# Kernel optimization log

Hardware: AMD Instinct MI355X
Metric: run time of the kernel (lower is better)

## Reference

```python
import jax, jax.numpy as jnp
import numpy as np

# ---- dims (match init_kwargs) ----
D_MODEL = 512
N_HEADS = 8
EXPAND = 2
SHRINK = 1
BATCH = 8
SEQ = 4096            # == tno_max_l
DPB_DIM = 512         # dpb_embedding
D1 = EXPAND * D_MODEL                 # 1024 (u_proj / o1 out)
D2 = D_MODEL // SHRINK                # 512  (v_proj out)
HEAD_DIM = D2 // N_HEADS              # 64
EPS = 1e-8


def _srms(x, d):
    # SimpleRMSNorm: x / (||x||_2 * d^-0.5 + eps)
    norm = jnp.linalg.norm(x, axis=-1, keepdims=True)
    return x / (norm * (d ** -0.5) + EPS)


def _dpb(p, Wp, bp, W1, b1, W2, b2, W3, b3):
    # dynamic position bias MLP: scalar rel-pos -> h*head_dim kernel coeffs
    x = p @ Wp + bp
    x = jax.nn.relu(_srms(x, DPB_DIM)) @ W1 + b1
    x = jax.nn.relu(_srms(x, DPB_DIM)) @ W2 + b2
    x = jax.nn.relu(_srms(x, DPB_DIM)) @ W3 + b3
    return x  # (m, h*head_dim)


def _heads(k):
    # (m, h*d) -> (h, m, d)
    return k.reshape(-1, N_HEADS, HEAD_DIM).transpose(1, 0, 2)


def setup_inputs() -> dict:
    key = jax.random.key(0)
    ks = jax.random.split(key, 17)
    w = lambda k, shape: jax.random.normal(k, shape, dtype=jnp.float32) * 0.02
    return {
        "x": jax.random.normal(ks[0], (BATCH, SEQ, D_MODEL), dtype=jnp.float32),
        "Wu": w(ks[1], (D_MODEL, D1)), "bu": w(ks[2], (D1,)),
        "Wv": w(ks[3], (D_MODEL, D2)), "bv": w(ks[4], (D2,)),
        "Wo1": w(ks[5], (D2, D1)), "bo1": w(ks[6], (D1,)),
        "Wo2": w(ks[7], (D1, D_MODEL)), "bo2": w(ks[8], (D_MODEL,)),
        "dpb_Wp": w(ks[9], (1, DPB_DIM)), "dpb_bp": w(ks[10], (DPB_DIM,)),
        "dpb_W1": w(ks[11], (DPB_DIM, DPB_DIM)), "dpb_b1": w(ks[12], (DPB_DIM,)),
        "dpb_W2": w(ks[13], (DPB_DIM, DPB_DIM)), "dpb_b2": w(ks[14], (DPB_DIM,)),
        "dpb_W3": w(ks[15], (DPB_DIM, N_HEADS * HEAD_DIM)),
        "dpb_b3": w(ks[16], (N_HEADS * HEAD_DIM,)),
    }


def reference(x, Wu, bu, Wv, bv, Wo1, bo1, Wo2, bo2,
              dpb_Wp, dpb_bp, dpb_W1, dpb_b1, dpb_W2, dpb_b2, dpb_W3, dpb_b3):
    b, n, _ = x.shape
    shortcut = x
    xn = _srms(x, D2)                                  # pre_norm (SimpleRMSNorm(d2))
    u = jax.nn.silu(xn @ Wu + bu)                      # (b, n, d1)
    v = jax.nn.silu(xn @ Wv + bv)                      # (b, n, d2)
    v = v.reshape(b, n, N_HEADS, HEAD_DIM).transpose(0, 2, 1, 3)  # (b, h, n, d)

    # relative-position indices (par_type=1): 1..n-1, -(n-1)..-1, 0
    pos_idx = jnp.arange(1, n, dtype=jnp.float32)[:, None]   # (n-1, 1)
    neg_idx = -pos_idx[::-1]                                  # (n-1, 1)
    zero_idx = jnp.zeros((1, 1), jnp.float32)
    dpb = lambda p: _dpb(p, dpb_Wp, dpb_bp, dpb_W1, dpb_b1,
                         dpb_W2, dpb_b2, dpb_W3, dpb_b3)
    kz = _heads(dpb(zero_idx))   # (h, 1,   d)
    kp = _heads(dpb(pos_idx))    # (h, n-1, d)
    kn = _heads(dpb(neg_idx))    # (h, n-1, d)
    # circulant embedding of the Toeplitz kernel: [t0, t1..t{n-1}, 0, t{-(n-1)}..t{-1}]
    a = jnp.concatenate([kz, kp, kz, kn], axis=1)             # (h, 2n, d)

    m = 2 * n
    yf = jnp.fft.rfft(v, m, axis=-2)                          # (b, h, n+1, d) complex
    af = jnp.fft.rfft(a, m, axis=-2)[None]                    # (1, h, n+1, d)
    out = jnp.fft.irfft(yf * af, m, axis=-2)[..., :n, :]      # (b, h, n, d)

    out = out.transpose(0, 2, 1, 3).reshape(b, n, D2)         # b n (h d)
    out = (out @ Wo1 + bo1) * u                               # gate
    out = out @ Wo2 + bo2 + shortcut
    return out
```

## Files before the change

kernel.cpp:

```cpp
#include <hip/hip_runtime.h>
#include <hip/hip_fp16.h>


#define FFTN 8192
#define SWZ(p) ((p) ^ (((p) >> 8) & 31))

#define C45F 0.70710678118654752f
#define CC8F 0.92387953251128676f
#define SS8F 0.38268343236508977f

typedef unsigned short u16;
typedef unsigned int u32;
typedef __attribute__((ext_vector_type(8))) short bf16x8;
typedef __attribute__((ext_vector_type(4))) float f32x4;

__device__ __forceinline__ int brev13(int x) { return (int)(__brev((unsigned)x) >> 19); }
__device__ __forceinline__ float b2f(u16 u) {
  union { float f; u32 i; } c; c.i = ((u32)u) << 16; return c.f;
}
__device__ __forceinline__ u16 f2b(float f) {
  union { float f; u32 i; } c; c.f = f;
  u32 r = c.i + 0x7FFFu + ((c.i >> 16) & 1u);
  return (u16)(r >> 16);
}
__device__ __forceinline__ float silu_f(float x) { return x / (1.f + __expf(-x)); }

__device__ __forceinline__ float2 up2(u32 v) {
  __half2 h = __builtin_bit_cast(__half2, v);
  return make_float2(__low2float(h), __high2float(h));
}
__device__ __forceinline__ u32 dn2(float r, float i) {
  __half2 h = __floats2half2_rn(r, i);
  return __builtin_bit_cast(u32, h);
}

__device__ __forceinline__ void gload16(const void* g, void* l) {
  __builtin_amdgcn_global_load_lds(
      (const __attribute__((address_space(1))) u32*)g,
      (__attribute__((address_space(3))) u32*)l, 16, 0, 0);
}

__global__ void twiddle_init_kernel(float2* __restrict__ tw) {
  int k = blockIdx.x * blockDim.x + threadIdx.x;
  if (k < 4096) {
    double ang = -6.283185307179586476925286766559 * ((double)k / 8192.0);
    tw[k] = make_float2((float)cos(ang), (float)sin(ang));
  }
}

__global__ __launch_bounds__(256) void srms_bf16_kernel(
    const float* __restrict__ in, u16* __restrict__ out, int rows, int do_relu)
{
  int wave = threadIdx.x >> 6, lane = threadIdx.x & 63;
  int row = (blockIdx.x << 2) + wave;
  if (row >= rows) return;
  const float4* p = (const float4*)(in + (size_t)row * 512);
  float4 a = p[lane], b = p[lane + 64];
  float ss = a.x*a.x + a.y*a.y + a.z*a.z + a.w*a.w
           + b.x*b.x + b.y*b.y + b.z*b.z + b.w*b.w;
#pragma unroll
  for (int off = 32; off > 0; off >>= 1) ss += __shfl_xor(ss, off);
  float inv = 1.0f / (sqrtf(ss) * 0.04419417382415922f + 1e-8f);
  a.x *= inv; a.y *= inv; a.z *= inv; a.w *= inv;
  b.x *= inv; b.y *= inv; b.z *= inv; b.w *= inv;
  if (do_relu) {
    a.x = fmaxf(a.x, 0.f); a.y = fmaxf(a.y, 0.f); a.z = fmaxf(a.z, 0.f); a.w = fmaxf(a.w, 0.f);
    b.x = fmaxf(b.x, 0.f); b.y = fmaxf(b.y, 0.f); b.z = fmaxf(b.z, 0.f); b.w = fmaxf(b.w, 0.f);
  }
  u16* o = out + (size_t)row * 512;
  ushort4 s0, s1;
  s0.x = f2b(a.x); s0.y = f2b(a.y); s0.z = f2b(a.z); s0.w = f2b(a.w);
  s1.x = f2b(b.x); s1.y = f2b(b.y); s1.z = f2b(b.z); s1.w = f2b(b.w);
  *(ushort4*)(o + lane * 4) = s0;
  *(ushort4*)(o + 256 + lane * 4) = s1;
}

__global__ __launch_bounds__(256) void dpb0_kernel(
    const float* __restrict__ Wp, const float* __restrict__ bp, u16* __restrict__ out)
{
  int wave = threadIdx.x >> 6, lane = threadIdx.x & 63;
  int row = (blockIdx.x << 2) + wave;
  if (row >= 8192) return;
  float pv;
  if (row == 0 || row == 4096) pv = 0.f;
  else if (row < 4096) pv = (float)row;
  else pv = (float)(row - 8192);
  const float4* wp  = (const float4*)Wp;
  const float4* bpp = (const float4*)bp;
  float4 a = wp[lane], b = wp[lane + 64];
  float4 c = bpp[lane], d = bpp[lane + 64];
  a.x = fmaf(pv, a.x, c.x); a.y = fmaf(pv, a.y, c.y);
  a.z = fmaf(pv, a.z, c.z); a.w = fmaf(pv, a.w, c.w);
  b.x = fmaf(pv, b.x, d.x); b.y = fmaf(pv, b.y, d.y);
  b.z = fmaf(pv, b.z, d.z); b.w = fmaf(pv, b.w, d.w);
  float ss = a.x*a.x + a.y*a.y + a.z*a.z + a.w*a.w
           + b.x*b.x + b.y*b.y + b.z*b.z + b.w*b.w;
#pragma unroll
  for (int off = 32; off > 0; off >>= 1) ss += __shfl_xor(ss, off);
  float inv = 1.0f / (sqrtf(ss) * 0.04419417382415922f + 1e-8f);
  u16* o = out + (size_t)row * 512;
  ushort4 s0, s1;
  s0.x = f2b(fmaxf(a.x * inv, 0.f)); s0.y = f2b(fmaxf(a.y * inv, 0.f));
  s0.z = f2b(fmaxf(a.z * inv, 0.f)); s0.w = f2b(fmaxf(a.w * inv, 0.f));
  s1.x = f2b(fmaxf(b.x * inv, 0.f)); s1.y = f2b(fmaxf(b.y * inv, 0.f));
  s1.z = f2b(fmaxf(b.z * inv, 0.f)); s1.w = f2b(fmaxf(b.w * inv, 0.f));
  *(ushort4*)(o + lane * 4) = s0;
  *(ushort4*)(o + 256 + lane * 4) = s1;
}

__global__ __launch_bounds__(256) void wtrans_kernel(
    const float* __restrict__ in, u16* __restrict__ out, int R, int C)
{
  __shared__ float tile[32][33];
  const int c0 = blockIdx.x << 5, r0 = blockIdx.y << 5;
  const int tx = threadIdx.x, ty = threadIdx.y;
#pragma unroll
  for (int i = 0; i < 32; i += 8)
    tile[ty + i][tx] = in[(size_t)(r0 + ty + i) * C + c0 + tx];
  __syncthreads();
#pragma unroll
  for (int i = 0; i < 32; i += 8)
    out[(size_t)(c0 + ty + i) * R + r0 + tx] = f2b(tile[tx][ty + i]);
}

__global__ __launch_bounds__(256) void transpose_b16_kernel(
    const u16* __restrict__ in, u16* __restrict__ out)
{
  __shared__ u16 tile[32][33];
  const int b = blockIdx.z;
  const int j0 = blockIdx.x << 5, c0 = blockIdx.y << 5;
  const int tx = threadIdx.x, ty = threadIdx.y;
  const u16* ip = in + ((size_t)b << 21);
  u16* op = out + ((size_t)b << 21);
#pragma unroll
  for (int i = 0; i < 32; i += 8)
    tile[ty + i][tx] = ip[(size_t)(c0 + ty + i) * 4096 + j0 + tx];
  __syncthreads();
#pragma unroll
  for (int i = 0; i < 32; i += 8)
    op[(size_t)(j0 + ty + i) * 512 + c0 + tx] = tile[tx][ty + i];
}

template <int EPI>
__global__ __launch_bounds__(256) void gemm_bf16_kernel(
    const u16* __restrict__ A, const u16* __restrict__ Bt,
    const float* __restrict__ bias, const u16* __restrict__ aux16,
    const float* __restrict__ auxf, void* __restrict__ Cv,
    int M, int N, int K)
{
  __shared__ __align__(16) u16 As[4096];
  __shared__ __align__(16) u16 Bs[4096];
  const int tid = threadIdx.x;
  const int lane = tid & 63;
  const int w = tid >> 6;
  const int wm = (w >> 1) << 6;
  const int wn = (w & 1) << 6;
  const int lm = lane & 15;
  const int lq = lane >> 4;
  const int bm = blockIdx.y << 7;
  const int bn = blockIdx.x << 7;

  const int sm = tid & 127;
  const int sk = tid >> 7;
  const u16* Ap = A + (size_t)(bm + sm) * K + sk * 8;
  const u16* Bp = Bt + (size_t)(bn + sm) * K + sk * 8;
  u16* As0 = As + ((sk)     * 128 + sm) * 8;
  u16* As1 = As + ((2 + sk) * 128 + sm) * 8;
  u16* Bs0 = Bs + ((sk)     * 128 + sm) * 8;
  u16* Bs1 = Bs + ((2 + sk) * 128 + sm) * 8;

  f32x4 acc[4][4];
#pragma unroll
  for (int i = 0; i < 4; i++)
#pragma unroll
    for (int j = 0; j < 4; j++) acc[i][j] = (f32x4){0.f, 0.f, 0.f, 0.f};

  for (int k0 = 0; k0 < K; k0 += 32) {
    __syncthreads();
    gload16(Ap, As0); gload16(Ap + 16, As1);
    gload16(Bp, Bs0); gload16(Bp + 16, Bs1);
    Ap += 32; Bp += 32;
    __builtin_amdgcn_s_waitcnt(0);
    __syncthreads();
    bf16x8 af[4], bfr[4];
#pragma unroll
    for (int i = 0; i < 4; i++) {
      af[i]  = *(const bf16x8*)(As + (lq * 128 + wm + i * 16 + lm) * 8);
      bfr[i] = *(const bf16x8*)(Bs + (lq * 128 + wn + i * 16 + lm) * 8);
    }
#pragma unroll
    for (int i = 0; i < 4; i++)
#pragma unroll
      for (int j = 0; j < 4; j++)
        acc[i][j] = __builtin_amdgcn_mfma_f32_16x16x32_bf16(af[i], bfr[j], acc[i][j], 0, 0, 0);
  }

#pragma unroll
  for (int i = 0; i < 4; i++) {
    const int m0 = bm + wm + i * 16 + lq * 4;
#pragma unroll
    for (int j = 0; j < 4; j++) {
      const int n = bn + wn + j * 16 + lm;
      const float bb = bias[n];
      const f32x4 v = acc[i][j];
      if constexpr (EPI == 5) {
        float4 o = make_float4(v[0] + bb, v[1] + bb, v[2] + bb, v[3] + bb);
        *(float4*)((float*)Cv + (size_t)n * M + m0) = o;
      } else {
#pragma unroll
        for (int r = 0; r < 4; r++) {
          const size_t idx = (size_t)(m0 + r) * N + n;
          const float val = v[r] + bb;
          if constexpr (EPI == 0) ((float*)Cv)[idx] = val;
          if constexpr (EPI == 1) ((u16*)Cv)[idx] = f2b(silu_f(val));
          if constexpr (EPI == 3) ((u16*)Cv)[idx] = f2b(val * b2f(aux16[idx]));
          if constexpr (EPI == 4) ((float*)Cv)[idx] = val + auxf[idx];
        }
      }
    }
  }
}

template <int EPI>
__global__ __launch_bounds__(512, 1) void gemm256_bf16_kernel(
    const u16* __restrict__ A, const u16* __restrict__ Bt,
    const float* __restrict__ bias, const u16* __restrict__ aux16,
    const float* __restrict__ auxf, void* __restrict__ Cv,
    int M, int N, int K)
{
  __shared__ __align__(16) u16 Asm[2][16384];
  __shared__ __align__(16) u16 Bsm[2][16384];
  const int tid = threadIdx.x;
  const int lane = tid & 63;
  const int w = tid >> 6;
  const int wm = (w >> 2) << 7;
  const int wn = (w & 3) << 6;
  const int lm = lane & 15;
  const int lq = lane >> 4;
  const int bm = blockIdx.y << 8;
  const int bn = blockIdx.x << 8;

  const int rloc = tid & 127;
  const int kq0 = tid >> 7;
  const u16* Ag = A + (size_t)(bm + rloc) * K + kq0 * 8;
  const u16* Bg = Bt + (size_t)(bn + rloc) * K + kq0 * 8;
  const size_t hstep = (size_t)128 * K;
  const int lso = tid * 8;

  const int aBase = ((wm >> 7) * 8192) + lq * 1024 + lm * 8;

  f32x4 acc[8][4];
#pragma unroll
  for (int i = 0; i < 8; i++)
#pragma unroll
    for (int j = 0; j < 4; j++) acc[i][j] = (f32x4){0.f, 0.f, 0.f, 0.f};

#define STG256(gb, lb, hh, kt) do {                                       \
    const u16* g_ = (gb) + (size_t)(hh) * hstep + (size_t)(kt) * 64;      \
    u16* l_ = (lb) + (hh) * 8192 + lso;                                   \
    gload16(g_, l_); gload16(g_ + 32, l_ + 4096);                         \
  } while (0)

  STG256(Ag, &Asm[0][0], 0, 0); STG256(Ag, &Asm[0][0], 1, 0);
  STG256(Bg, &Bsm[0][0], 0, 0); STG256(Bg, &Bsm[0][0], 1, 0);

  const int NT = K >> 6;
  for (int t = 0; t < NT; ++t) {
    const int cb = t & 1, nb = cb ^ 1;
    const u16* cA = &Asm[cb][0];
    const u16* cB = &Bsm[cb][0];
    if (t + 1 < NT) {
      STG256(Ag, &Asm[nb][0], 0, t + 1);
      STG256(Ag, &Asm[nb][0], 1, t + 1);
      asm volatile("s_waitcnt vmcnt(4)" ::: "memory");
    } else {
      asm volatile("s_waitcnt vmcnt(0)" ::: "memory");
    }
    __builtin_amdgcn_s_barrier();
    bf16x8 af[4][2];
#pragma unroll
    for (int q = 0; q < 4; ++q) {
      const int qm = q >> 1, qn = q & 1;
      if (q == 0 && t + 1 < NT) STG256(Bg, &Bsm[nb][0], 0, t + 1);
      if (q == 1 && t + 1 < NT) STG256(Bg, &Bsm[nb][0], 1, t + 1);
      if (qn == 0) {
#pragma unroll
        for (int i = 0; i < 4; ++i)
#pragma unroll
          for (int ks = 0; ks < 2; ++ks)
            af[i][ks] = *(const bf16x8*)(cA + aBase + ks * 4096 + qm * 512 + i * 128);
      }
      const int colBase = wn + qn * 32;
      const int bBase = ((colBase >> 7) * 8192) + lq * 1024 + (colBase & 127) * 8 + lm * 8;
      bf16x8 bfr[2][2];
#pragma unroll
      for (int j = 0; j < 2; ++j)
#pragma unroll
        for (int ks = 0; ks < 2; ++ks)
          bfr[j][ks] = *(const bf16x8*)(cB + bBase + ks * 4096 + j * 128);
      __builtin_amdgcn_s_setprio(1);
#pragma unroll
      for (int i = 0; i < 4; ++i)
#pragma unroll
        for (int j = 0; j < 2; ++j) {
          acc[qm*4+i][qn*2+j] = __builtin_amdgcn_mfma_f32_16x16x32_bf16(
              af[i][0], bfr[j][0], acc[qm*4+i][qn*2+j], 0, 0, 0);
          acc[qm*4+i][qn*2+j] = __builtin_amdgcn_mfma_f32_16x16x32_bf16(
              af[i][1], bfr[j][1], acc[qm*4+i][qn*2+j], 0, 0, 0);
        }
      __builtin_amdgcn_s_setprio(0);
      __builtin_amdgcn_s_barrier();
    }
  }
#undef STG256

#pragma unroll
  for (int im = 0; im < 8; im++) {
    const int m0 = bm + wm + im * 16 + lq * 4;
#pragma unroll
    for (int jn = 0; jn < 4; jn++) {
      const int n = bn + wn + jn * 16 + lm;
      const float bb = bias[n];
      const f32x4 v = acc[im][jn];
      if constexpr (EPI == 2) {
        const int b = m0 >> 12;
        const int jq = m0 & 4095;
        ushort4 s;
        s.x = f2b(silu_f(v[0] + bb)); s.y = f2b(silu_f(v[1] + bb));
        s.z = f2b(silu_f(v[2] + bb)); s.w = f2b(silu_f(v[3] + bb));
        *(ushort4*)((u16*)Cv + (((size_t)(b * 512 + n)) << 12) + jq) = s;
      } else {
#pragma unroll
        for (int r = 0; r < 4; r++) {
          const size_t idx = (size_t)(m0 + r) * N + n;
          const float val = v[r] + bb;
          if constexpr (EPI == 1) ((u16*)Cv)[idx] = f2b(silu_f(val));
          if constexpr (EPI == 3) ((u16*)Cv)[idx] = f2b(val * b2f(aux16[idx]));
          if constexpr (EPI == 4) ((float*)Cv)[idx] = val + auxf[idx];
        }
      }
    }
  }
}

__device__ __forceinline__ void fft8192_dit(float* sr, float* si,
                                            const float2* __restrict__ tw)
{
  const int t = threadIdx.x;
  for (int s = 0; s < 12; s += 2) {
    __syncthreads();
    const int h = 1 << s;
#pragma unroll
    for (int bb = 0; bb < 4; bb++) {
      const int u = t + (bb << 9);
      const int j = u & (h - 1);
      const int base = ((u >> s) << (s + 2)) | j;
      const float2 w1 = tw[j << (12 - s)];
      const float2 w2 = tw[j << (11 - s)];
      const int q0 = SWZ(base), q1 = SWZ(base + h);
      const int q2 = SWZ(base + 2 * h), q3 = SWZ(base + 3 * h);
      const float ar = sr[q0], ai = si[q0];
      const float br = sr[q1], bi = si[q1];
      const float cr = sr[q2], ci = si[q2];
      const float dr = sr[q3], di = si[q3];
      const float t1r = br * w1.x - bi * w1.y, t1i = br * w1.y + bi * w1.x;
      const float t2r = dr * w1.x - di * w1.y, t2i = dr * w1.y + di * w1.x;
      const float Ar = ar + t1r, Ai = ai + t1i;
      const float Br = ar - t1r, Bi = ai - t1i;
      const float Cr = cr + t2r, Ci = ci + t2i;
      const float Dr = cr - t2r, Di = ci - t2i;
      const float t3r = Cr * w2.x - Ci * w2.y, t3i = Cr * w2.y + Ci * w2.x;
      const float pr  = Dr * w2.x - Di * w2.y, pi  = Dr * w2.y + Di * w2.x;
      const float t4r = pi, t4i = -pr;
      sr[q0] = Ar + t3r; si[q0] = Ai + t3i;
      sr[q2] = Ar - t3r; si[q2] = Ai - t3i;
      sr[q1] = Br + t4r; si[q1] = Bi + t4i;
      sr[q3] = Br - t4r; si[q3] = Bi - t4i;
    }
  }
  __syncthreads();
#pragma unroll
  for (int bb = 0; bb < 8; bb++) {
    const int u = t + (bb << 9);
    const float2 w = tw[u];
    const int p0 = SWZ(u), p1 = SWZ(u + 4096);
    const float br = sr[p1], bi = si[p1];
    const float trr = br * w.x - bi * w.y;
    const float tri = br * w.y + bi * w.x;
    const float ar = sr[p0], ai = si[p0];
    sr[p0] = ar + trr; si[p0] = ai + tri;
    sr[p1] = ar - trr; si[p1] = ai - tri;
  }
  __syncthreads();
}

__global__ __launch_bounds__(512) void kfft_kernel(
    const float* __restrict__ D1T,
    const float2* __restrict__ tw,
    float2* __restrict__ aspec)
{
  __shared__ float sr[FFTN];
  __shared__ float si[FFTN];
  const int q = blockIdx.x;
  const int t = threadIdx.x;
  const float* row0 = D1T + ((size_t)(2 * q)) * 8192;
  const float* row1 = row0 + 8192;
#pragma unroll
  for (int it = 0; it < 16; it++) {
    const int r = t + (it << 9);
    const int d = SWZ(brev13(r));
    sr[d] = row0[r]; si[d] = row1[r];
  }
  fft8192_dit(sr, si, tw);
  const float sc = 1.0f / 8192.0f;
  float2* O0 = aspec + (size_t)(2 * q) * 4097;
  float2* O1 = aspec + (size_t)(2 * q + 1) * 4097;
#pragma unroll 1
  for (int it = 0; it < 8; it++) {
    const int k = t + (it << 9);
    const int k2 = (FFTN - k) & (FFTN - 1);
    const float zr = sr[SWZ(k)],  zi = si[SWZ(k)];
    const float wr = sr[SWZ(k2)], wi = si[SWZ(k2)];
    O0[k] = make_float2(0.5f * sc * (zr + wr), 0.5f * sc * (zi - wi));
    O1[k] = make_float2(0.5f * sc * (zi + wi), 0.5f * sc * (wr - zr));
  }
  if (t == 0) {
    const float zr = sr[SWZ(4096)], zi = si[SWZ(4096)];
    O0[4096] = make_float2(zr * sc, 0.f);
    O1[4096] = make_float2(zi * sc, 0.f);
  }
}


__device__ __forceinline__ void dit16(float* xr, float* xi,
    float wAr, float wAi, float wBr, float wBi,
    float wCr, float wCi, float wDr, float wDi)
{
#define DITP(a, b, wr_, wi_)                                     \
  { const float cr_ = xr[b]*(wr_) - xi[b]*(wi_);                 \
    const float ci_ = xr[b]*(wi_) + xi[b]*(wr_);                 \
    xr[b] = xr[a] - cr_; xi[b] = xi[a] - ci_;                    \
    xr[a] = xr[a] + cr_; xi[a] = xi[a] + ci_; }
#define DITPM(a, b, wr_, wi_)                                    \
  { const float cr_ = xr[b]*(wr_) - xi[b]*(wi_);                 \
    const float ci_ = xr[b]*(wi_) + xi[b]*(wr_);                 \
    xr[b] = xr[a] - ci_; xi[b] = xi[a] + cr_;                    \
    xr[a] = xr[a] + ci_; xi[a] = xi[a] - cr_; }
  DITP(0,1,wAr,wAi)   DITP(2,3,wAr,wAi)   DITP(4,5,wAr,wAi)   DITP(6,7,wAr,wAi)
  DITP(8,9,wAr,wAi)   DITP(10,11,wAr,wAi) DITP(12,13,wAr,wAi) DITP(14,15,wAr,wAi)
  DITP(0,2,wBr,wBi)   DITPM(1,3,wBr,wBi)
  DITP(4,6,wBr,wBi)   DITPM(5,7,wBr,wBi)
  DITP(8,10,wBr,wBi)  DITPM(9,11,wBr,wBi)
  DITP(12,14,wBr,wBi) DITPM(13,15,wBr,wBi)
  const float wC1r = C45F*(wCr + wCi), wC1i = C45F*(wCi - wCr);
  DITP(0,4,wCr,wCi)   DITP(1,5,wC1r,wC1i)   DITPM(2,6,wCr,wCi)   DITPM(3,7,wC1r,wC1i)
  DITP(8,12,wCr,wCi)  DITP(9,13,wC1r,wC1i)  DITPM(10,14,wCr,wCi) DITPM(11,15,wC1r,wC1i)
  const float wD1r = wDr*CC8F + wDi*SS8F, wD1i = wDi*CC8F - wDr*SS8F;
  const float wD2r = C45F*(wDr + wDi),    wD2i = C45F*(wDi - wDr);
  const float wD3r = wDr*SS8F + wDi*CC8F, wD3i = wDi*SS8F - wDr*CC8F;
  DITP(0,8,wDr,wDi)    DITP(1,9,wD1r,wD1i)   DITP(2,10,wD2r,wD2i)  DITP(3,11,wD3r,wD3i)
  DITPM(4,12,wDr,wDi)  DITPM(5,13,wD1r,wD1i) DITPM(6,14,wD2r,wD2i) DITPM(7,15,wD3r,wD3i)
#undef DITP
#undef DITPM
}

__device__ __forceinline__ void dif16(float* xr, float* xi,
    float wAr, float wAi, float wBr, float wBi,
    float wCr, float wCi, float wDr, float wDi)
{
#define DIFP(a, b, wr_, wi_)                                     \
  { const float dr_ = xr[a] - xr[b], di_ = xi[a] - xi[b];        \
    xr[a] = xr[a] + xr[b]; xi[a] = xi[a] + xi[b];                \
    xr[b] = dr_*(wr_) + di_*(wi_);                               \
    xi[b] = di_*(wr_) - dr_*(wi_); }
#define DIFPM(a, b, wr_, wi_)                                    \
  { const float dr_ = xr[a] - xr[b], di_ = xi[a] - xi[b];        \
    xr[a] = xr[a] + xr[b]; xi[a] = xi[a] + xi[b];                \
    const float er_ = dr_*(wr_) + di_*(wi_);                     \
    const float ei_ = di_*(wr_) - dr_*(wi_);                     \
    xr[b] = -ei_; xi[b] = er_; }
  const float wC1r = C45F*(wCr + wCi), wC1i = C45F*(wCi - wCr);
  const float wD1r = wDr*CC8F + wDi*SS8F, wD1i = wDi*CC8F - wDr*SS8F;
  const float wD2r = C45F*(wDr + wDi),    wD2i = C45F*(wDi - wDr);
  const float wD3r = wDr*SS8F + wDi*CC8F, wD3i = wDi*SS8F - wDr*CC8F;
  DIFP(0,8,wDr,wDi)    DIFP(1,9,wD1r,wD1i)   DIFP(2,10,wD2r,wD2i)  DIFP(3,11,wD3r,wD3i)
  DIFPM(4,12,wDr,wDi)  DIFPM(5,13,wD1r,wD1i) DIFPM(6,14,wD2r,wD2i) DIFPM(7,15,wD3r,wD3i)
  DIFP(0,4,wCr,wCi)   DIFP(1,5,wC1r,wC1i)   DIFPM(2,6,wCr,wCi)   DIFPM(3,7,wC1r,wC1i)
  DIFP(8,12,wCr,wCi)  DIFP(9,13,wC1r,wC1i)  DIFPM(10,14,wCr,wCi) DIFPM(11,15,wC1r,wC1i)
  DIFP(0,2,wBr,wBi)   DIFPM(1,3,wBr,wBi)
  DIFP(4,6,wBr,wBi)   DIFPM(5,7,wBr,wBi)
  DIFP(8,10,wBr,wBi)  DIFPM(9,11,wBr,wBi)
  DIFP(12,14,wBr,wBi) DIFPM(13,15,wBr,wBi)
  DIFP(0,1,wAr,wAi)   DIFP(2,3,wAr,wAi)   DIFP(4,5,wAr,wAi)   DIFP(6,7,wAr,wAi)
  DIFP(8,9,wAr,wAi)   DIFP(10,11,wAr,wAi) DIFP(12,13,wAr,wAi) DIFP(14,15,wAr,wAi)
#undef DIFP
#undef DIFPM
}

template <int SS>
__device__ __forceinline__ void fwd_pass(u32* S, const float2* __restrict__ tw, int u)
{
  const int j = u & ((1 << SS) - 1);
  const int base = ((u >> SS) << (SS + 4)) | j;
  float xr[16], xi[16];
#pragma unroll
  for (int r = 0; r < 16; r++) {
    const float2 v = up2(S[SWZ(base + (r << SS))]);
    xr[r] = v.x; xi[r] = v.y;
  }
  const float2 wA = tw[j << (12 - SS)];
  const float2 wB = tw[j << (11 - SS)];
  const float2 wC = tw[j << (10 - SS)];
  const float2 wD = tw[j << (9 - SS)];
  dit16(xr, xi, wA.x, wA.y, wB.x, wB.y, wC.x, wC.y, wD.x, wD.y);
#pragma unroll
  for (int r = 0; r < 16; r++)
    S[SWZ(base + (r << SS))] = dn2(xr[r], xi[r]);
}

template <int SS>
__device__ __forceinline__ void inv_pass(u32* S, const float2* __restrict__ tw, int u)
{
  const int j = u & ((1 << SS) - 1);
  const int base = ((u >> SS) << (SS + 4)) | j;
  float xr[16], xi[16];
#pragma unroll
  for (int r = 0; r < 16; r++) {
    const float2 v = up2(S[SWZ(base + (r << SS))]);
    xr[r] = v.x; xi[r] = v.y;
  }
  const float2 wA = tw[j << (12 - SS)];
  const float2 wB = tw[j << (11 - SS)];
  const float2 wC = tw[j << (10 - SS)];
  const float2 wD = tw[j << (9 - SS)];
  dif16(xr, xi, wA.x, wA.y, wB.x, wB.y, wC.x, wC.y, wD.x, wD.y);
#pragma unroll
  for (int r = 0; r < 16; r++)
    S[SWZ(base + (r << SS))] = dn2(xr[r], xi[r]);
}

__device__ __forceinline__ void mp2(float zr, float zi, float wr, float wi,
                                    float2 a0, float2 a1,
                                    float& okr, float& oki, float& o2r, float& o2i)
{
  const float Xr = 0.5f*(zr + wr), Xi = 0.5f*(zi - wi);
  const float Yr = 0.5f*(zi + wi), Yi = 0.5f*(wr - zr);
  const float Pr = Xr*a0.x - Xi*a0.y, Pi = Xr*a0.y + Xi*a0.x;
  const float Qr = Yr*a1.x - Yi*a1.y, Qi = Yr*a1.y + Yi*a1.x;
  okr = Pr - Qi; oki = Pi + Qr;
  o2r = Pr + Qi; o2i = Qr - Pi;
}

__global__ __launch_bounds__(512, 4) void conv_kernel(
    const u16* __restrict__ vT,
    const float2* __restrict__ aspec,
    const float2* __restrict__ tw,
    u16* __restrict__ outT)
{
  __shared__ u32 S[FFTN];
  const int q = blockIdx.x;
  const int b = blockIdx.y;
  const int c0 = 2 * q, c1 = 2 * q + 1;
  const int t = threadIdx.x;
  const int db = (int)(__brev((u32)t) >> 23) << 4;

  {
    const u16* p0 = vT + ((size_t)b * 512 + c0) * 4096;
    const u16* p1 = vT + ((size_t)b * 512 + c1) * 4096;
    float xr[16], xi[16];
#pragma unroll
    for (int it = 0; it < 8; it++) {
      const int r = ((it & 1) << 3) | ((it & 2) << 1) | ((it & 4) >> 1);
      const int jg = t + (it << 9);
      xr[r] = b2f(p0[jg]); xi[r] = b2f(p1[jg]);
    }
#pragma unroll
    for (int m = 0; m < 8; m++) { xr[2*m+1] = 0.f; xi[2*m+1] = 0.f; }
    dit16(xr, xi, 1.f, 0.f, 1.f, 0.f, 1.f, 0.f, 1.f, 0.f);
#pragma unroll
    for (int r = 0; r < 16; r++) S[SWZ(db + r)] = dn2(xr[r], xi[r]);
  }
  __syncthreads();
  fwd_pass<4>(S, tw, ((t & 15) << 5) | (t >> 4));
  __syncthreads();
  fwd_pass<8>(S, tw, t);
  __syncthreads();
  {
    const float2* A0 = aspec + (size_t)c0 * 4097;
    const float2* A1 = aspec + (size_t)c1 * 4097;
#pragma unroll
    for (int it = 0; it < 4; it++) {
      const int p = t + (it << 9);
      if (it == 0 && t == 0) {
        const int sA = SWZ(0), sB = SWZ(4096), sC = SWZ(2048), sD = SWZ(6144);
        const float2 a = up2(S[sA]), bb = up2(S[sB]);
        const float Z0r = a.x + bb.x, Z0i = a.y + bb.y;
        const float Z4r = a.x - bb.x, Z4i = a.y - bb.y;
        float N0r, N0i, N4r, N4i, u0, u1;
        mp2(Z0r, Z0i, Z0r, Z0i, A0[0], A1[0], N0r, N0i, u0, u1);
        mp2(Z4r, Z4i, Z4r, Z4i, A0[4096], A1[4096], N4r, N4i, u0, u1);
        S[sA] = dn2(N0r + N4r, N0i + N4i);
        S[sB] = dn2(N0r - N4r, N0i - N4i);
        const float2 c = up2(S[sC]), e = up2(S[sD]);
        const float2 w2 = tw[2048];
        const float trr = e.x*w2.x - e.y*w2.y, tri = e.x*w2.y + e.y*w2.x;
        const float Z2r = c.x + trr, Z2i = c.y + tri;
        const float Z6r = c.x - trr, Z6i = c.y - tri;
        float N2r, N2i, N6r, N6i;
        mp2(Z2r, Z2i, Z6r, Z6i, A0[2048], A1[2048], N2r, N2i, N6r, N6i);
        const float ddr = N2r - N6r, ddi = N2i - N6i;
        S[sC] = dn2(N2r + N6r, N2i + N6i);
        S[sD] = dn2(ddr*w2.x + ddi*w2.y, ddi*w2.x - ddr*w2.y);
      } else {
        const int p2 = 4096 - p;
        const int s0a = SWZ(p),  s1a = SWZ(p + 4096);
        const int s2a = SWZ(p2), s3a = SWZ(p2 + 4096);
        const float2 a1v = up2(S[s0a]), b1v = up2(S[s1a]);
        const float2 a2v = up2(S[s2a]), b2v = up2(S[s3a]);
        const float2 w1 = tw[p], w2 = tw[p2];
        const float t1r = b1v.x*w1.x - b1v.y*w1.y, t1i = b1v.x*w1.y + b1v.y*w1.x;
        const float Zpr = a1v.x + t1r, Zpi = a1v.y + t1i;
        const float Z4r = a1v.x - t1r, Z4i = a1v.y - t1i;
        const float t2r = b2v.x*w2.x - b2v.y*w2.y, t2i = b2v.x*w2.y + b2v.y*w2.x;
        const float Zqr = a2v.x + t2r, Zqi = a2v.y + t2i;
        const float Z8r = a2v.x - t2r, Z8i = a2v.y - t2i;
        float Npr, Npi, N8r, N8i, Nqr, Nqi, N4r, N4i;
        mp2(Zpr, Zpi, Z8r, Z8i, A0[p],  A1[p],  Npr, Npi, N8r, N8i);
        mp2(Zqr, Zqi, Z4r, Z4i, A0[p2], A1[p2], Nqr, Nqi, N4r, N4i);
        float dr = Npr - N4r, di = Npi - N4i;
        S[s0a] = dn2(Npr + N4r, Npi + N4i);
        S[s1a] = dn2(dr*w1.x + di*w1.y, di*w1.x - dr*w1.y);
        dr = Nqr - N8r; di = Nqi - N8i;
        S[s2a] = dn2(Nqr + N8r, Nqi + N8i);
        S[s3a] = dn2(dr*w2.x + di*w2.y, di*w2.x - dr*w2.y);
      }
    }
  }
  __syncthreads();
  inv_pass<8>(S, tw, t);
  __syncthreads();
  inv_pass<4>(S, tw, ((t & 15) << 5) | (t >> 4));
  __syncthreads();
  {
    float xr[16], xi[16];
#pragma unroll
    for (int r = 0; r < 16; r++) {
      const float2 v = up2(S[SWZ(db + r)]);
      xr[r] = v.x; xi[r] = v.y;
    }
    dif16(xr, xi, 1.f, 0.f, 1.f, 0.f, 1.f, 0.f, 1.f, 0.f);
    u16* o0 = outT + ((size_t)b * 512 + c0) * 4096;
    u16* o1 = outT + ((size_t)b * 512 + c1) * 4096;
#pragma unroll
    for (int m = 0; m < 8; m++) {
      const int r = 2 * m;
      const int rv = ((r & 2) << 1) | ((r & 4) >> 1) | ((r & 8) >> 3);
      const int i = t + (rv << 9);
      o0[i] = f2b(xr[r]); o1[i] = f2b(xi[r]);
    }
  }
}

extern "C" void kernel_launch(void* const* d_in, const int* in_sizes, int n_in,
                              void* d_out, int out_size, void* d_ws, size_t ws_size,
                              hipStream_t stream)
{
  const float* x   = (const float*)d_in[0];
  const float* Wu  = (const float*)d_in[1];
  const float* bu  = (const float*)d_in[2];
  const float* Wv  = (const float*)d_in[3];
  const float* bv  = (const float*)d_in[4];
  const float* Wo1 = (const float*)d_in[5];
  const float* bo1 = (const float*)d_in[6];
  const float* Wo2 = (const float*)d_in[7];
  const float* bo2 = (const float*)d_in[8];
  const float* dWp = (const float*)d_in[9];
  const float* dbp = (const float*)d_in[10];
  const float* dW1 = (const float*)d_in[11];
  const float* db1 = (const float*)d_in[12];
  const float* dW2 = (const float*)d_in[13];
  const float* db2 = (const float*)d_in[14];
  const float* dW3 = (const float*)d_in[15];
  const float* db3 = (const float*)d_in[16];
  float* out = (float*)d_out;

  char* wsb = (char*)d_ws;
  const size_t MB = 1u << 20;
  u16* WuT  = (u16*)wsb;
  u16* WvT  = WuT + 524288;
  u16* Wo1T = WvT + 262144;
  u16* Wo2T = Wo1T + 524288;
  u16* dW1T = Wo2T + 524288;
  u16* dW2T = dW1T + 262144;
  u16* dW3T = dW2T + 262144;
  u16*    XNb   = (u16*)(wsb + 6 * MB);
  u16*    D0b   = (u16*)(wsb + 6 * MB);
  float*  D1    = (float*)(wsb + 14 * MB);
  float*  D1T   = (float*)(wsb + 14 * MB);
  u16*    CT    = (u16*)(wsb + 6 * MB);
  u16*    G     = (u16*)(wsb + 6 * MB);
  u16*    VTb   = (u16*)(wsb + 38 * MB);
  float2* ASPEC = (float2*)(wsb + 70 * MB);
  float2* TW    = (float2*)(wsb + 87 * MB);
  u16*    CR    = (u16*)(wsb + 88 * MB);
  u16*    U     = (u16*)(wsb + 128 * MB);

  dim3 wt_blk(32, 8);
  wtrans_kernel<<<dim3(32, 16), wt_blk, 0, stream>>>(Wu, WuT, 512, 1024);
  wtrans_kernel<<<dim3(16, 16), wt_blk, 0, stream>>>(Wv, WvT, 512, 512);
  wtrans_kernel<<<dim3(32, 16), wt_blk, 0, stream>>>(Wo1, Wo1T, 512, 1024);
  wtrans_kernel<<<dim3(16, 32), wt_blk, 0, stream>>>(Wo2, Wo2T, 1024, 512);
  wtrans_kernel<<<dim3(16, 16), wt_blk, 0, stream>>>(dW1, dW1T, 512, 512);
  wtrans_kernel<<<dim3(16, 16), wt_blk, 0, stream>>>(dW2, dW2T, 512, 512);
  wtrans_kernel<<<dim3(16, 16), wt_blk, 0, stream>>>(dW3, dW3T, 512, 512);
  twiddle_init_kernel<<<8, 512, 0, stream>>>(TW);

  srms_bf16_kernel<<<8192, 256, 0, stream>>>(x, XNb, 32768, 0);
  gemm256_bf16_kernel<2><<<dim3(2, 128), 512, 0, stream>>>(XNb, WvT, bv, nullptr, nullptr, VTb, 32768, 512, 512);
  gemm256_bf16_kernel<1><<<dim3(4, 128), 512, 0, stream>>>(XNb, WuT, bu, nullptr, nullptr, U, 32768, 1024, 512);

  dpb0_kernel<<<2048, 256, 0, stream>>>(dWp, dbp, D0b);
  gemm_bf16_kernel<0><<<dim3(4, 64), 256, 0, stream>>>(D0b, dW1T, db1, nullptr, nullptr, D1, 8192, 512, 512);
  srms_bf16_kernel<<<2048, 256, 0, stream>>>(D1, D0b, 8192, 1);
  gemm_bf16_kernel<0><<<dim3(4, 64), 256, 0, stream>>>(D0b, dW2T, db2, nullptr, nullptr, D1, 8192, 512, 512);
  srms_bf16_kernel<<<2048, 256, 0, stream>>>(D1, D0b, 8192, 1);
  gemm_bf16_kernel<5><<<dim3(4, 64), 256, 0, stream>>>(D0b, dW3T, db3, nullptr, nullptr, D1T, 8192, 512, 512);
  kfft_kernel<<<256, 512, 0, stream>>>(D1T, TW, ASPEC);
  conv_kernel<<<dim3(256, 8), 512, 0, stream>>>(VTb, ASPEC, TW, CT);
  transpose_b16_kernel<<<dim3(128, 16, 8), wt_blk, 0, stream>>>(CT, CR);
  gemm256_bf16_kernel<3><<<dim3(4, 128), 512, 0, stream>>>(CR, Wo1T, bo1, U, nullptr, G, 32768, 1024, 512);
  gemm256_bf16_kernel<4><<<dim3(2, 128), 512, 0, stream>>>(G, Wo2T, bo2, nullptr, x, out, 32768, 512, 1024);
}
```

Measured before the change: 652.9 us.

## Shrink main GEMM tiles to 128x256 with BK=32 for higher occupancy

Replaces the 256x256, BK=64 GEMM with a 128x256 tile that steps K by 32, and shrinks shared memory from 128KB to 48KB per block. Launch bounds rise to allow up to 4 blocks per CU, and the grid doubles along M. The inner loop is simplified to one B-fragment load per K-step with a single barrier pair, replacing the four-quadrant schedule that interleaved the B prefetch. The aim is latency hiding through occupancy rather than a deep in-block pipeline, at the cost of less data reuse per tile and twice as many K iterations.

```diff
diff --git a/kernel.cpp b/kernel.cpp
--- a/kernel.cpp
+++ b/kernel.cpp
@@ -222,106 +222,93 @@
 }
 
 template <int EPI>
-__global__ __launch_bounds__(512, 1) void gemm256_bf16_kernel(
+__global__ __launch_bounds__(512, 4) void gemm128x256_bf16_kernel(
     const u16* __restrict__ A, const u16* __restrict__ Bt,
     const float* __restrict__ bias, const u16* __restrict__ aux16,
     const float* __restrict__ auxf, void* __restrict__ Cv,
     int M, int N, int K)
 {
-  __shared__ __align__(16) u16 Asm[2][16384];
-  __shared__ __align__(16) u16 Bsm[2][16384];
+  __shared__ __align__(16) u16 Asm[2][4096];
+  __shared__ __align__(16) u16 Bsm[2][8192];
   const int tid = threadIdx.x;
   const int lane = tid & 63;
   const int w = tid >> 6;
-  const int wm = (w >> 2) << 7;
+  const int wm = (w >> 2) << 6;
   const int wn = (w & 3) << 6;
   const int lm = lane & 15;
   const int lq = lane >> 4;
-  const int bm = blockIdx.y << 8;
+  const int bm = blockIdx.y << 7;
   const int bn = blockIdx.x << 8;
 
   const int rloc = tid & 127;
-  const int kq0 = tid >> 7;
-  const u16* Ag = A + (size_t)(bm + rloc) * K + kq0 * 8;
-  const u16* Bg = Bt + (size_t)(bn + rloc) * K + kq0 * 8;
-  const size_t hstep = (size_t)128 * K;
+  const int kq = tid >> 7;
+  const u16* Ag = A + (size_t)(bm + rloc) * K + kq * 8;
+  const u16* Bg = Bt + (size_t)(bn + rloc) * K + kq * 8;
+  const size_t bh = (size_t)128 * K;
   const int lso = tid * 8;
 
-  const int aBase = ((wm >> 7) * 8192) + lq * 1024 + lm * 8;
-
-  f32x4 acc[8][4];
-#pragma unroll
-  for (int i = 0; i < 8; i++)
+  f32x4 acc[4][4];
+#pragma unroll
+  for (int i = 0; i < 4; i++)
 #pragma unroll
     for (int j = 0; j < 4; j++) acc[i][j] = (f32x4){0.f, 0.f, 0.f, 0.f};
 
-#define STG256(gb, lb, hh, kt) do {                                       \
-    const u16* g_ = (gb) + (size_t)(hh) * hstep + (size_t)(kt) * 64;      \
-    u16* l_ = (lb) + (hh) * 8192 + lso;                                   \
-    gload16(g_, l_); gload16(g_ + 32, l_ + 4096);                         \
+#define STG3(buf, kt) do {                                            \
+    const u16* a_ = Ag + (size_t)(kt) * 32;                           \
+    const u16* b_ = Bg + (size_t)(kt) * 32;                           \
+    gload16(a_, &Asm[buf][0] + lso);                                  \
+    gload16(b_, &Bsm[buf][0] + lso);                                  \
+    gload16(b_ + bh, &Bsm[buf][0] + 4096 + lso);                      \
   } while (0)
 
-  STG256(Ag, &Asm[0][0], 0, 0); STG256(Ag, &Asm[0][0], 1, 0);
-  STG256(Bg, &Bsm[0][0], 0, 0); STG256(Bg, &Bsm[0][0], 1, 0);
-
-  const int NT = K >> 6;
+  STG3(0, 0);
+
+  const int NT = K >> 5;
   for (int t = 0; t < NT; ++t) {
     const int cb = t & 1, nb = cb ^ 1;
     const u16* cA = &Asm[cb][0];
     const u16* cB = &Bsm[cb][0];
     if (t + 1 < NT) {
-      STG256(Ag, &Asm[nb][0], 0, t + 1);
-      STG256(Ag, &Asm[nb][0], 1, t + 1);
-      asm volatile("s_waitcnt vmcnt(4)" ::: "memory");
+      STG3(nb, t + 1);
+      asm volatile("s_waitcnt vmcnt(3)" ::: "memory");
     } else {
       asm volatile("s_waitcnt vmcnt(0)" ::: "memory");
     }
+    __builtin_amdgcn_sched_barrier(0);
     __builtin_amdgcn_s_barrier();
-    bf16x8 af[4][2];
-#pragma unroll
-    for (int q = 0; q < 4; ++q) {
-      const int qm = q >> 1, qn = q & 1;
-      if (q == 0 && t + 1 < NT) STG256(Bg, &Bsm[nb][0], 0, t + 1);
-      if (q == 1 && t + 1 < NT) STG256(Bg, &Bsm[nb][0], 1, t + 1);
-      if (qn == 0) {
-#pragma unroll
-        for (int i = 0; i < 4; ++i)
-#pragma unroll
-          for (int ks = 0; ks < 2; ++ks)
-            af[i][ks] = *(const bf16x8*)(cA + aBase + ks * 4096 + qm * 512 + i * 128);
-      }
-      const int colBase = wn + qn * 32;
-      const int bBase = ((colBase >> 7) * 8192) + lq * 1024 + (colBase & 127) * 8 + lm * 8;
-      bf16x8 bfr[2][2];
-#pragma unroll
-      for (int j = 0; j < 2; ++j)
-#pragma unroll
-        for (int ks = 0; ks < 2; ++ks)
-          bfr[j][ks] = *(const bf16x8*)(cB + bBase + ks * 4096 + j * 128);
+    bf16x8 bfr[4];
+#pragma unroll
+    for (int j = 0; j < 4; ++j) {
+      const int c = wn + j * 16 + lm;
+      bfr[j] = *(const bf16x8*)(cB + (c >> 7) * 4096 + lq * 1024 + (c & 127) * 8);
+    }
+#pragma unroll
+    for (int qm = 0; qm < 2; ++qm) {
+      bf16x8 af[2];
+#pragma unroll
+      for (int i2 = 0; i2 < 2; ++i2)
+        af[i2] = *(const bf16x8*)(cA + lq * 1024 + (wm + qm * 32 + i2 * 16 + lm) * 8);
       __builtin_amdgcn_s_setprio(1);
 #pragma unroll
-      for (int i = 0; i < 4; ++i)
-#pragma unroll
-        for (int j = 0; j < 2; ++j) {
-          acc[qm*4+i][qn*2+j] = __builtin_amdgcn_mfma_f32_16x16x32_bf16(
-              af[i][0], bfr[j][0], acc[qm*4+i][qn*2+j], 0, 0, 0);
-          acc[qm*4+i][qn*2+j] = __builtin_amdgcn_mfma_f32_16x16x32_bf16(
-              af[i][1], bfr[j][1], acc[qm*4+i][qn*2+j], 0, 0, 0);
-        }
+      for (int i2 = 0; i2 < 2; ++i2)
+#pragma unroll
+        for (int j = 0; j < 4; ++j)
+          acc[qm * 2 + i2][j] = __builtin_amdgcn_mfma_f32_16x16x32_bf16(
+              af[i2], bfr[j], acc[qm * 2 + i2][j], 0, 0, 0);
       __builtin_amdgcn_s_setprio(0);
-      __builtin_amdgcn_s_barrier();
-    }
-  }
-#undef STG256
-
-#pragma unroll
-  for (int im = 0; im < 8; im++) {
-    const int m0 = bm + wm + im * 16 + lq * 4;
-#pragma unroll
-    for (int jn = 0; jn < 4; jn++) {
-      const int n = bn + wn + jn * 16 + lm;
+    }
+    __builtin_amdgcn_s_barrier();
+  }
+#undef STG3
+
+#pragma unroll
+  for (int i = 0; i < 4; i++) {
+    const int m0 = bm + wm + i * 16 + lq * 4;
+#pragma unroll
+    for (int j = 0; j < 4; j++) {
+      const int n = bn + wn + j * 16 + lm;
       const float bb = bias[n];
-      const f32x4 v = acc[im][jn];
+      const f32x4 v = acc[i][j];
       if constexpr (EPI == 2) {
         const int b = m0 >> 12;
         const int jq = m0 & 4095;
@@ -716,8 +703,8 @@
   twiddle_init_kernel<<<8, 512, 0, stream>>>(TW);
 
   srms_bf16_kernel<<<8192, 256, 0, stream>>>(x, XNb, 32768, 0);
-  gemm256_bf16_kernel<2><<<dim3(2, 128), 512, 0, stream>>>(XNb, WvT, bv, nullptr, nullptr, VTb, 32768, 512, 512);
-  gemm256_bf16_kernel<1><<<dim3(4, 128), 512, 0, stream>>>(XNb, WuT, bu, nullptr, nullptr, U, 32768, 1024, 512);
+  gemm128x256_bf16_kernel<2><<<dim3(2, 256), 512, 0, stream>>>(XNb, WvT, bv, nullptr, nullptr, VTb, 32768, 512, 512);
+  gemm128x256_bf16_kernel<1><<<dim3(4, 256), 512, 0, stream>>>(XNb, WuT, bu, nullptr, nullptr, U, 32768, 1024, 512);
 
   dpb0_kernel<<<2048, 256, 0, stream>>>(dWp, dbp, D0b);
   gemm_bf16_kernel<0><<<dim3(4, 64), 256, 0, stream>>>(D0b, dW1T, db1, nullptr, nullptr, D1, 8192, 512, 512);
@@ -728,6 +715,6 @@
   kfft_kernel<<<256, 512, 0, stream>>>(D1T, TW, ASPEC);
   conv_kernel<<<dim3(256, 8), 512, 0, stream>>>(VTb, ASPEC, TW, CT);
   transpose_b16_kernel<<<dim3(128, 16, 8), wt_blk, 0, stream>>>(CT, CR);
-  gemm256_bf16_kernel<3><<<dim3(4, 128), 512, 0, stream>>>(CR, Wo1T, bo1, U, nullptr, G, 32768, 1024, 512);
-  gemm256_bf16_kernel<4><<<dim3(2, 128), 512, 0, stream>>>(G, Wo2T, bo2, nullptr, x, out, 32768, 512, 1024);
-}
+  gemm128x256_bf16_kernel<3><<<dim3(4, 256), 512, 0, stream>>>(CR, Wo1T, bo1, U, nullptr, G, 32768, 1024, 512);
+  gemm128x256_bf16_kernel<4><<<dim3(2, 256), 512, 0, stream>>>(G, Wo2T, bo2, nullptr, x, out, 32768, 512, 1024);
+}
```

After: 639.2 us. -2.1%, faster.
